# Optimization experiments

Hardware: AMD Instinct MI355X
Metric: run time of the kernel (lower is better)

Reference implementation:

```python
import jax, jax.numpy as jnp
import numpy as np

N, E = 20000, 320000
D_IN, HID, HEADS, OUT = 256, 64, 8, 64
K1 = int(np.ceil(0.75 * N))   # 15000 nodes after pool1
K2 = int(np.ceil(0.75 * K1))  # 11250 nodes after pool2
NEG = -1e30


def setup_inputs():
    key = jax.random.key(0)
    ks = jax.random.split(key, 24)
    s = 0.1
    rn = lambda k, shape: jax.random.normal(k, shape, jnp.float32) * s
    HH = HEADS * HID  # 512
    p = {}
    p["x"] = jax.random.normal(ks[0], (N, D_IN), jnp.float32)
    p["edge_index"] = jax.random.randint(ks[1], (2, E), 0, N, dtype=jnp.int32)
    # gat1: GATv2Conv(D_IN -> HID, heads=HEADS), concat output dim HH
    p["g1_wl"] = rn(ks[2], (D_IN, HH)); p["g1_wr"] = rn(ks[3], (D_IN, HH))
    p["g1_att"] = rn(ks[4], (HEADS, HID)); p["g1_b"] = jnp.zeros((HH,), jnp.float32)
    # pool1 scoring GNN: GATConv(HH -> 1, heads=1) + SelectTopK weight
    p["p1_w"] = rn(ks[5], (HH, 1)); p["p1_asrc"] = rn(ks[6], (1,)); p["p1_adst"] = rn(ks[7], (1,))
    p["p1_b"] = jnp.zeros((1,), jnp.float32); p["p1_sel"] = rn(ks[8], (1,)) + 0.5
    # gat2: GATv2Conv(HH -> HID, heads=1)
    p["g2_wl"] = rn(ks[9], (HH, HID)); p["g2_wr"] = rn(ks[10], (HH, HID))
    p["g2_att"] = rn(ks[11], (1, HID)); p["g2_b"] = jnp.zeros((HID,), jnp.float32)
    # pool2 scoring GNN: GATConv(HID -> 1)
    p["p2_w"] = rn(ks[12], (HID, 1)); p["p2_asrc"] = rn(ks[13], (1,)); p["p2_adst"] = rn(ks[14], (1,))
    p["p2_b"] = jnp.zeros((1,), jnp.float32); p["p2_sel"] = rn(ks[15], (1,)) + 0.5
    # MLP head
    p["l1_w"] = rn(ks[16], (2 * HH, HH)); p["l1_b"] = jnp.zeros((HH,), jnp.float32)
    d2 = OUT * (HEADS // 2); d3 = OUT * (HEADS // 4)
    p["l2_w"] = rn(ks[17], (HH, d2)); p["l2_b"] = jnp.zeros((d2,), jnp.float32)
    p["l3_w"] = rn(ks[18], (d2, d3)); p["l3_b"] = jnp.zeros((d3,), jnp.float32)
    p["l4_w"] = rn(ks[19], (d3, 2)); p["l4_b"] = jnp.zeros((2,), jnp.float32)
    return p


def _seg_softmax(e, dst, valid, n):
    # numerically stable segment softmax over destination nodes; invalid edges -> 0
    e = jnp.where(valid[:, None], e, NEG)
    m = jax.ops.segment_max(e, dst, num_segments=n)
    ex = jnp.exp(e - m[dst])
    ex = jnp.where(valid[:, None], ex, 0.0)
    den = jax.ops.segment_sum(ex, dst, num_segments=n)
    return ex / den[dst]


def gatv2(x, src, dst, valid, wl, wr, att, b):
    # GATv2Conv: score = att . LeakyReLU(Wl x_src + Wr x_dst), segment softmax, concat heads
    n = x.shape[0]
    h, c = att.shape
    xl = (x @ wl).reshape(n, h, c)
    xr = (x @ wr).reshape(n, h, c)
    loop = jnp.arange(n, dtype=src.dtype)  # add_self_loops=True
    s = jnp.concatenate([src, loop]); d = jnp.concatenate([dst, loop])
    v = jnp.concatenate([valid, jnp.ones((n,), bool)])
    m = jax.nn.leaky_relu(xl[s] + xr[d], 0.2)          # [E', H, C]
    e = jnp.einsum("ehc,hc->eh", m, att)               # [E', H]
    a = _seg_softmax(e, d, v, n)
    out = jax.ops.segment_sum(a[..., None] * xl[s], d, num_segments=n)
    return out.reshape(n, h * c) + b


def gat_score(x, src, dst, valid, w, asrc, adst, b):
    # GATConv(in -> 1, heads=1): per-node scalar projection score
    n = x.shape[0]
    xl = x @ w                                          # [n, 1]
    al = (xl * asrc).sum(-1); ar = (xl * adst).sum(-1)  # [n]
    loop = jnp.arange(n, dtype=src.dtype)
    s = jnp.concatenate([src, loop]); d = jnp.concatenate([dst, loop])
    v = jnp.concatenate([valid, jnp.ones((n,), bool)])
    e = jax.nn.leaky_relu(al[s] + ar[d], 0.2)[:, None]
    a = _seg_softmax(e, d, v, n)
    return jax.ops.segment_sum(a * xl[s], d, num_segments=n) + b


def sag_pool(x, src, dst, valid, k, w, asrc, adst, b, sel_w):
    # SAGPooling: GNN score -> tanh -> top-k -> x[perm]*score, edge filtering via mask
    attn = gat_score(x, src, dst, valid, w, asrc, adst, b)           # [n, 1]
    score = jnp.tanh((attn * sel_w).sum(-1) / jnp.linalg.norm(sel_w))  # SelectTopK
    vals, perm = jax.lax.top_k(score, k)
    xp = x[perm] * vals[:, None]
    new_id = jnp.full((x.shape[0],), -1, src.dtype).at[perm].set(jnp.arange(k, dtype=src.dtype))
    s2, d2 = new_id[src], new_id[dst]
    v2 = valid & (s2 >= 0) & (d2 >= 0)
    return xp, jnp.where(v2, s2, 0), jnp.where(v2, d2, 0), v2


def _forward(x, edge_index, g1_wl, g1_wr, g1_att, g1_b, p1_w, p1_asrc, p1_adst, p1_b, p1_sel,
             g2_wl, g2_wr, g2_att, g2_b, p2_w, p2_asrc, p2_adst, p2_b, p2_sel,
             l1_w, l1_b, l2_w, l2_b, l3_w, l3_b, l4_w, l4_b):
    src, dst = edge_index[0], edge_index[1]
    valid = jnp.ones((src.shape[0],), bool)
    h = jax.nn.relu(gatv2(x, src, dst, valid, g1_wl, g1_wr, g1_att, g1_b))
    h, s1, d1, v1 = sag_pool(h, src, dst, valid, K1, p1_w, p1_asrc, p1_adst, p1_b, p1_sel)
    # single graph -> global pools are plain reductions over nodes
    x1 = jnp.concatenate([h.max(0, keepdims=True), h.mean(0, keepdims=True)], axis=1)
    h2 = jax.nn.relu(gatv2(h, s1, d1, v1, g2_wl, g2_wr, g2_att, g2_b))
    h2, _, _, _ = sag_pool(h2, s1, d1, v1, K2, p2_w, p2_asrc, p2_adst, p2_b, p2_sel)
    gmax = jnp.tile(h2.max(0, keepdims=True), (1, HEADS))
    gmean = jnp.tile(h2.mean(0, keepdims=True), (1, HEADS))
    z = x1 + jnp.concatenate([gmax, gmean], axis=1)
    z = jax.nn.relu(z @ l1_w + l1_b)   # dropout is identity at eval
    z = jax.nn.relu(z @ l2_w + l2_b)
    z = jax.nn.relu(z @ l3_w + l3_b)
    logits = z @ l4_w + l4_b
    return logits, jax.nn.softmax(logits, axis=-1)


def reference(x, edge_index, g1_wl, g1_wr, g1_att, g1_b, p1_w, p1_asrc, p1_adst, p1_b, p1_sel,
              g2_wl, g2_wr, g2_att, g2_b, p2_w, p2_asrc, p2_adst, p2_b, p2_sel,
              l1_w, l1_b, l2_w, l2_b, l3_w, l3_b, l4_w, l4_b):
    return _forward(x, edge_index, g1_wl, g1_wr, g1_att, g1_b, p1_w, p1_asrc, p1_adst, p1_b, p1_sel,
                    g2_wl, g2_wr, g2_att, g2_b, p2_w, p2_asrc, p2_adst, p2_b, p2_sel,
                    l1_w, l1_b, l2_w, l2_b, l3_w, l3_b, l4_w, l4_b)
```

## Files before the change

### kernel.cpp

```cpp
#include <hip/hip_runtime.h>
#include <math.h>

#define N_NODES 20000
#define E_EDGES 320000
#define DIN     256
#define HHD     512
#define HIDD    64
#define NHEADS  8
#define K1N     15000
#define K2N     11250

typedef unsigned short u16;
typedef __attribute__((ext_vector_type(8))) short bf16x8;
typedef __attribute__((ext_vector_type(4))) float f32x4;

static inline int cdiv(long long a, long long b) { return (int)((a + b - 1) / b); }

__device__ __forceinline__ void atomicMaxF(float* addr, float val) {
  int* ai = (int*)addr;
  int old = __float_as_int(*addr);
  while (__int_as_float(old) < val) {
    int assumed = old;
    old = atomicCAS(ai, assumed, __float_as_int(val));
    if (old == assumed) break;
  }
}

__device__ __forceinline__ u16 f2bf(float x) {
  unsigned u = __float_as_uint(x);
  return (u16)((u + 0x7FFFu + ((u >> 16) & 1u)) >> 16);
}
__device__ __forceinline__ float bfval(u16 b) { return __uint_as_float(((unsigned)b) << 16); }

__global__ void init_all(int* deg1, int* rank1, float* pools) {
  int i = blockIdx.x * blockDim.x + threadIdx.x;
  if (i < N_NODES) deg1[i] = 0;
  else if (i < 2 * N_NODES) rank1[i - N_NODES] = 0;
  else {
    int idx = i - 2 * N_NODES;
    if (idx < 1152)
      pools[idx] = (idx < 512 || (idx >= 1024 && idx < 1088)) ? -INFINITY : 0.f;
  }
}

__global__ void conv_fused(const float* __restrict__ A, const int* __restrict__ perm,
                           const float* __restrict__ scalev,
                           u16* __restrict__ ah, u16* __restrict__ al, int M, int K,
                           const float* __restrict__ w1, const float* __restrict__ w2,
                           u16* __restrict__ wh, u16* __restrict__ wl, int ncHalf,
                           int aBlocks) {
  if ((int)blockIdx.x < aBlocks) {
    long long i = (long long)blockIdx.x * blockDim.x + threadIdx.x;
    long long e0 = i * 4;
    if (e0 >= (long long)M * K) return;
    int row = (int)(e0 / K), col = (int)(e0 % K);
    int ar = perm ? perm[row] : row;
    float4 v = *(const float4*)(A + (size_t)ar * K + col);
    if (scalev) { float s = scalev[ar]; v.x *= s; v.y *= s; v.z *= s; v.w *= s; }
    u16 h0 = f2bf(v.x), h1 = f2bf(v.y), h2 = f2bf(v.z), h3 = f2bf(v.w);
    u16 l0 = f2bf(v.x - bfval(h0)), l1 = f2bf(v.y - bfval(h1));
    u16 l2 = f2bf(v.z - bfval(h2)), l3 = f2bf(v.w - bfval(h3));
    uint2 hp, lp;
    hp.x = (unsigned)h0 | ((unsigned)h1 << 16); hp.y = (unsigned)h2 | ((unsigned)h3 << 16);
    lp.x = (unsigned)l0 | ((unsigned)l1 << 16); lp.y = (unsigned)l2 | ((unsigned)l3 << 16);
    *(uint2*)(ah + e0) = hp;
    *(uint2*)(al + e0) = lp;
  } else {
    int i = (blockIdx.x - aBlocks) * blockDim.x + threadIdx.x;
    int NT = 2 * ncHalf;
    if (i >= NT * K) return;
    int n = i % NT, k = i / NT;
    float v = (n < ncHalf) ? w1[(size_t)k * ncHalf + n] : w2[(size_t)k * ncHalf + (n - ncHalf)];
    u16 h = f2bf(v);
    u16 l = f2bf(v - bfval(h));
    wh[(size_t)n * K + k] = h;
    wl[(size_t)n * K + k] = l;
  }
}

template<int BT>
__global__ __launch_bounds__(256) void gemm_bf16x3(const u16* __restrict__ ah,
                                                   const u16* __restrict__ al,
                                                   const u16* __restrict__ wh,
                                                   const u16* __restrict__ wl,
                                                   float* __restrict__ c1,
                                                   float* __restrict__ c2,
                                                   int M, int K, int ncHalf) {
  constexpr int F = BT / 32;
  __shared__ u16 Ah[BT][40], Al[BT][40], Bh[BT][40], Bl[BT][40];
  int tid = threadIdx.x;
  int lane = tid & 63, wid = tid >> 6;
  int wr = (wid >> 1) * (BT / 2), wc = (wid & 1) * (BT / 2);
  int brow = blockIdx.y * BT, bcol = blockIdx.x * BT;
  int fr = lane & 15, kg = lane >> 4;
  f32x4 acc[F][F];
#pragma unroll
  for (int i = 0; i < F; i++)
#pragma unroll
    for (int j = 0; j < F; j++) acc[i][j] = (f32x4){0.f, 0.f, 0.f, 0.f};

  for (int k0 = 0; k0 < K; k0 += 32) {
    constexpr int ITER = (BT * 32) / (256 * 8);
#pragma unroll
    for (int i = 0; i < ITER; i++) {
      int pos = tid + i * 256;
      int row = pos >> 2;
      int kc = (pos & 3) * 8;
      int gr = brow + row;
      float4 z = make_float4(0.f, 0.f, 0.f, 0.f);
      float4 vah = (gr < M) ? *(const float4*)(ah + (size_t)gr * K + k0 + kc) : z;
      float4 val = (gr < M) ? *(const float4*)(al + (size_t)gr * K + k0 + kc) : z;
      *(float4*)(&Ah[row][kc]) = vah;
      *(float4*)(&Al[row][kc]) = val;
      int gn = bcol + row;
      *(float4*)(&Bh[row][kc]) = *(const float4*)(wh + (size_t)gn * K + k0 + kc);
      *(float4*)(&Bl[row][kc]) = *(const float4*)(wl + (size_t)gn * K + k0 + kc);
    }
    __syncthreads();
    bf16x8 fa_h[F], fa_l[F], fb_h[F], fb_l[F];
#pragma unroll
    for (int t = 0; t < F; t++) {
      fa_h[t] = *(const bf16x8*)(&Ah[wr + t * 16 + fr][kg * 8]);
      fa_l[t] = *(const bf16x8*)(&Al[wr + t * 16 + fr][kg * 8]);
      fb_h[t] = *(const bf16x8*)(&Bh[wc + t * 16 + fr][kg * 8]);
      fb_l[t] = *(const bf16x8*)(&Bl[wc + t * 16 + fr][kg * 8]);
    }
#pragma unroll
    for (int i = 0; i < F; i++)
#pragma unroll
      for (int j = 0; j < F; j++) {
        acc[i][j] = __builtin_amdgcn_mfma_f32_16x16x32_bf16(fa_h[i], fb_h[j], acc[i][j], 0, 0, 0);
        acc[i][j] = __builtin_amdgcn_mfma_f32_16x16x32_bf16(fa_h[i], fb_l[j], acc[i][j], 0, 0, 0);
        acc[i][j] = __builtin_amdgcn_mfma_f32_16x16x32_bf16(fa_l[i], fb_h[j], acc[i][j], 0, 0, 0);
      }
    __syncthreads();
  }
#pragma unroll
  for (int i = 0; i < F; i++) {
    int r0 = brow + wr + i * 16 + kg * 4;
#pragma unroll
    for (int j = 0; j < F; j++) {
      int cg = bcol + wc + j * 16 + fr;
      float* cp = (cg < ncHalf) ? c1 : c2;
      int cc = (cg < ncHalf) ? cg : cg - ncHalf;
#pragma unroll
      for (int r = 0; r < 4; r++) {
        int gr = r0 + r;
        if (gr < M) cp[(size_t)gr * ncHalf + cc] = acc[i][j][r];
      }
    }
  }
}

__global__ void deg_count(const int* __restrict__ src, const int* __restrict__ dst,
                          const int* __restrict__ newid, int* __restrict__ deg,
                          int nloops) {
  int i = blockIdx.x * blockDim.x + threadIdx.x;
  if (i >= E_EDGES + nloops) return;
  int d;
  if (i < E_EDGES) {
    if (newid) {
      int s = newid[src[i]]; d = newid[dst[i]];
      if (s < 0 || d < 0) return;
    } else d = dst[i];
  } else d = i - E_EDGES;
  atomicAdd(&deg[d], 1);
}

__global__ __launch_bounds__(1024) void scan_excl(const int* deg, int* rowptr,
                                                  int* cursor, int n) {
  __shared__ int wsum[16];
  __shared__ int carry;
  int tid = threadIdx.x, lane = tid & 63, wid = tid >> 6;
  if (tid == 0) { carry = 0; rowptr[0] = 0; }
  __syncthreads();
  for (int base = 0; base < n; base += 1024) {
    int v = (base + tid < n) ? deg[base + tid] : 0;
    int s = v;
#pragma unroll
    for (int off = 1; off < 64; off <<= 1) {
      int t = __shfl_up(s, off);
      if (lane >= off) s += t;
    }
    if (lane == 63) wsum[wid] = s;
    __syncthreads();
    if (wid == 0) {
      int w = (lane < 16) ? wsum[lane] : 0;
#pragma unroll
      for (int off = 1; off < 16; off <<= 1) {
        int t = __shfl_up(w, off);
        if (lane >= off) w += t;
      }
      if (lane < 16) wsum[lane] = w;
    }
    __syncthreads();
    int incl = s + (wid > 0 ? wsum[wid - 1] : 0) + carry;
    if (base + tid < n) { rowptr[base + tid + 1] = incl; cursor[base + tid] = incl - v; }
    __syncthreads();
    if (tid == 1023) carry = incl;
    __syncthreads();
  }
}

__global__ void csr_scatter(const int* __restrict__ src, const int* __restrict__ dst,
                            const int* __restrict__ newid, int* __restrict__ cursor,
                            int* __restrict__ csr_s, int nloops) {
  int i = blockIdx.x * blockDim.x + threadIdx.x;
  if (i >= E_EDGES + nloops) return;
  int s, d;
  if (i < E_EDGES) {
    s = src[i]; d = dst[i];
    if (newid) {
      s = newid[s]; d = newid[d];
      if (s < 0 || d < 0) return;
    }
  } else s = d = i - E_EDGES;
  int pos = atomicAdd(&cursor[d], 1);
  csr_s[pos] = s;
}

__global__ __launch_bounds__(256) void gat1_fused(const int* __restrict__ rowptr,
                                                  const int* __restrict__ csr_s,
                                                  const float* __restrict__ xl,
                                                  const float* __restrict__ xr,
                                                  const float* __restrict__ att,
                                                  const float* __restrict__ bias,
                                                  const float* __restrict__ pw,
                                                  float* __restrict__ out,
                                                  float* __restrict__ xls) {
  int lane = threadIdx.x & 63;
  long long t = (long long)blockIdx.x * blockDim.x + threadIdx.x;
  int d = (int)(t >> 6);
  if (d >= N_NODES) return;
  int base = lane * 8;
  float4 a0 = *(const float4*)(att + base);
  float4 a1 = *(const float4*)(att + base + 4);
  const float* xrp = xr + (size_t)d * HHD + base;
  float4 r0 = *(const float4*)(xrp);
  float4 r1 = *(const float4*)(xrp + 4);
  float m = -INFINITY, den = 0.f;
  float acc[8] = {0.f, 0.f, 0.f, 0.f, 0.f, 0.f, 0.f, 0.f};
  int b0 = rowptr[d];
  int cnt = rowptr[d + 1] - b0;
  const int* sp = csr_s + b0;

  auto online = [&](float4 v0, float4 v1) {
    float p, tv;
    tv = v0.x + r0.x; tv = tv > 0.f ? tv : 0.2f * tv; p  = tv * a0.x;
    tv = v0.y + r0.y; tv = tv > 0.f ? tv : 0.2f * tv; p += tv * a0.y;
    tv = v0.z + r0.z; tv = tv > 0.f ? tv : 0.2f * tv; p += tv * a0.z;
    tv = v0.w + r0.w; tv = tv > 0.f ? tv : 0.2f * tv; p += tv * a0.w;
    tv = v1.x + r1.x; tv = tv > 0.f ? tv : 0.2f * tv; p += tv * a1.x;
    tv = v1.y + r1.y; tv = tv > 0.f ? tv : 0.2f * tv; p += tv * a1.y;
    tv = v1.z + r1.z; tv = tv > 0.f ? tv : 0.2f * tv; p += tv * a1.z;
    tv = v1.w + r1.w; tv = tv > 0.f ? tv : 0.2f * tv; p += tv * a1.w;
    p += __shfl_xor(p, 1); p += __shfl_xor(p, 2); p += __shfl_xor(p, 4);
    float nm = fmaxf(m, p);
    float w  = __expf(p - nm);
    float sc = __expf(m - nm);
    den = den * sc + w;
    acc[0] = acc[0] * sc + w * v0.x;
    acc[1] = acc[1] * sc + w * v0.y;
    acc[2] = acc[2] * sc + w * v0.z;
    acc[3] = acc[3] * sc + w * v0.w;
    acc[4] = acc[4] * sc + w * v1.x;
    acc[5] = acc[5] * sc + w * v1.y;
    acc[6] = acc[6] * sc + w * v1.z;
    acc[7] = acc[7] * sc + w * v1.w;
    m = nm;
  };

  float4 A0, A1, B0, B1, C0, C1, D0, D1;
  float4 zz = make_float4(0.f, 0.f, 0.f, 0.f);
  {
    const float* p0 = xl + (size_t)sp[0] * HHD + base;
    A0 = *(const float4*)p0; A1 = *(const float4*)(p0 + 4);
  }
  B0 = zz; B1 = zz; C0 = zz; C1 = zz; D0 = zz; D1 = zz;
  if (cnt > 1) { const float* p = xl + (size_t)sp[1] * HHD + base; B0 = *(const float4*)p; B1 = *(const float4*)(p + 4); }
  if (cnt > 2) { const float* p = xl + (size_t)sp[2] * HHD + base; C0 = *(const float4*)p; C1 = *(const float4*)(p + 4); }
  if (cnt > 3) { const float* p = xl + (size_t)sp[3] * HHD + base; D0 = *(const float4*)p; D1 = *(const float4*)(p + 4); }
  int j = 0;
  for (; j + 4 <= cnt; j += 4) {
    float4 v0 = A0, v1 = A1;
    if (j + 4 < cnt) { const float* p = xl + (size_t)sp[j + 4] * HHD + base; A0 = *(const float4*)p; A1 = *(const float4*)(p + 4); }
    online(v0, v1);
    v0 = B0; v1 = B1;
    if (j + 5 < cnt) { const float* p = xl + (size_t)sp[j + 5] * HHD + base; B0 = *(const float4*)p; B1 = *(const float4*)(p + 4); }
    online(v0, v1);
    v0 = C0; v1 = C1;
    if (j + 6 < cnt) { const float* p = xl + (size_t)sp[j + 6] * HHD + base; C0 = *(const float4*)p; C1 = *(const float4*)(p + 4); }
    online(v0, v1);
    v0 = D0; v1 = D1;
    if (j + 7 < cnt) { const float* p = xl + (size_t)sp[j + 7] * HHD + base; D0 = *(const float4*)p; D1 = *(const float4*)(p + 4); }
    online(v0, v1);
  }
  if (j < cnt) {
    online(A0, A1);
    if (j + 1 < cnt) {
      online(B0, B1);
      if (j + 2 < cnt) online(C0, C1);
    }
  }

  float inv = 1.f / den;
  float4 b0v = *(const float4*)(bias + base);
  float4 b1v = *(const float4*)(bias + base + 4);
  float o[8];
  o[0] = acc[0] * inv + b0v.x; o[1] = acc[1] * inv + b0v.y;
  o[2] = acc[2] * inv + b0v.z; o[3] = acc[3] * inv + b0v.w;
  o[4] = acc[4] * inv + b1v.x; o[5] = acc[5] * inv + b1v.y;
  o[6] = acc[6] * inv + b1v.z; o[7] = acc[7] * inv + b1v.w;
#pragma unroll
  for (int k = 0; k < 8; k++) o[k] = o[k] > 0.f ? o[k] : 0.f;
  float* op = out + (size_t)d * HHD + base;
  *(float4*)(op)     = make_float4(o[0], o[1], o[2], o[3]);
  *(float4*)(op + 4) = make_float4(o[4], o[5], o[6], o[7]);
  float4 w0 = *(const float4*)(pw + base);
  float4 w1 = *(const float4*)(pw + base + 4);
  float sdot = o[0]*w0.x + o[1]*w0.y + o[2]*w0.z + o[3]*w0.w
             + o[4]*w1.x + o[5]*w1.y + o[6]*w1.z + o[7]*w1.w;
#pragma unroll
  for (int off = 32; off > 0; off >>= 1) sdot += __shfl_xor(sdot, off);
  if (lane == 0) xls[d] = sdot;
}

__global__ __launch_bounds__(256) void gat2_fused(const int* __restrict__ rowptr,
                                                  const int* __restrict__ csr_s,
                                                  const float* __restrict__ xl,
                                                  const float* __restrict__ xr,
                                                  const float* __restrict__ att,
                                                  const float* __restrict__ bias,
                                                  const float* __restrict__ pw,
                                                  float* __restrict__ out,
                                                  float* __restrict__ xls, int n) {
  int lane = threadIdx.x & 63;
  long long t = (long long)blockIdx.x * blockDim.x + threadIdx.x;
  int d = (int)(t >> 6);
  if (d >= n) return;
  float av = att[lane];
  float rr = xr[(size_t)d * HIDD + lane];
  float m = -INFINITY, den = 0.f, acc = 0.f;
  int b0 = rowptr[d];
  int cnt = rowptr[d + 1] - b0;
  const int* sp = csr_s + b0;

  auto online = [&](float v) {
    float tv = v + rr; tv = tv > 0.f ? tv : 0.2f * tv;
    float p = tv * av;
#pragma unroll
    for (int off = 32; off > 0; off >>= 1) p += __shfl_xor(p, off);
    float nm = fmaxf(m, p);
    float w  = __expf(p - nm);
    float sc = __expf(m - nm);
    den = den * sc + w;
    acc = acc * sc + w * v;
    m = nm;
  };

  float vA = xl[(size_t)sp[0] * HIDD + lane];
  float vB = (cnt > 1) ? xl[(size_t)sp[1] * HIDD + lane] : 0.f;
  float vC = (cnt > 2) ? xl[(size_t)sp[2] * HIDD + lane] : 0.f;
  float vD = (cnt > 3) ? xl[(size_t)sp[3] * HIDD + lane] : 0.f;
  int j = 0;
  for (; j + 4 <= cnt; j += 4) {
    float v = vA;
    if (j + 4 < cnt) vA = xl[(size_t)sp[j + 4] * HIDD + lane];
    online(v);
    v = vB;
    if (j + 5 < cnt) vB = xl[(size_t)sp[j + 5] * HIDD + lane];
    online(v);
    v = vC;
    if (j + 6 < cnt) vC = xl[(size_t)sp[j + 6] * HIDD + lane];
    online(v);
    v = vD;
    if (j + 7 < cnt) vD = xl[(size_t)sp[j + 7] * HIDD + lane];
    online(v);
  }
  if (j < cnt) {
    online(vA);
    if (j + 1 < cnt) {
      online(vB);
      if (j + 2 < cnt) online(vC);
    }
  }

  float o = acc / den + bias[lane];
  o = o > 0.f ? o : 0.f;
  out[(size_t)d * HIDD + lane] = o;
  float sdot = o * pw[lane];
#pragma unroll
  for (int off = 32; off > 0; off >>= 1) sdot += __shfl_xor(sdot, off);
  if (lane == 0) xls[d] = sdot;
}

__global__ __launch_bounds__(256) void pool_score(const int* __restrict__ rowptr,
                                                  const int* __restrict__ csr_s,
                                                  const float* __restrict__ xls,
                                                  const float* __restrict__ asrc,
                                                  const float* __restrict__ adst,
                                                  const float* __restrict__ bias,
                                                  const float* __restrict__ sel,
                                                  float* __restrict__ score, int n) {
  int d = blockIdx.x * blockDim.x + threadIdx.x;
  if (d >= n) return;
  float as = asrc[0], ad = adst[0];
  float ar = xls[d] * ad;
  int b0 = rowptr[d];
  int cnt = rowptr[d + 1] - b0;
  const int* sp = csr_s + b0;
  float m = -INFINITY, den = 0.f, num = 0.f;
  auto upd = [&](float xs) {
    float e = xs * as + ar;
    e = e > 0.f ? e : 0.2f * e;
    float nm = fmaxf(m, e);
    float scv = __expf(m - nm);
    float ex = __expf(e - nm);
    den = den * scv + ex;
    num = num * scv + ex * xs;
    m = nm;
  };
  float xA = xls[sp[0]];
  float xB = (cnt > 1) ? xls[sp[1]] : 0.f;
  float xC = (cnt > 2) ? xls[sp[2]] : 0.f;
  float xD = (cnt > 3) ? xls[sp[3]] : 0.f;
  int j = 0;
  for (; j + 4 <= cnt; j += 4) {
    float x1 = xA;
    if (j + 4 < cnt) xA = xls[sp[j + 4]];
    upd(x1);
    float x2 = xB;
    if (j + 5 < cnt) xB = xls[sp[j + 5]];
    upd(x2);
    float x3 = xC;
    if (j + 6 < cnt) xC = xls[sp[j + 6]];
    upd(x3);
    float x4 = xD;
    if (j + 7 < cnt) xD = xls[sp[j + 7]];
    upd(x4);
  }
  if (j < cnt) {
    upd(xA);
    if (j + 1 < cnt) {
      upd(xB);
      if (j + 2 < cnt) upd(xC);
    }
  }
  float attn = num / den + bias[0];
  float sv = sel[0];
  score[d] = tanhf(attn * sv / fabsf(sv));
}

#define TK_CHUNK 512
__global__ __launch_bounds__(256) void topk_count(const float* __restrict__ score,
                                                  int* __restrict__ rank, int n,
                                                  int* __restrict__ zbuf, int zn) {
  __shared__ float sc[TK_CHUNK];
  if (zbuf) {
    long long fid = ((long long)blockIdx.y * gridDim.x + blockIdx.x) * 256 + threadIdx.x;
    if (fid < zn) zbuf[fid] = 0;
  }
  int i = blockIdx.x * 256 + threadIdx.x;
  int base = blockIdx.y * TK_CHUNK;
  int cnt = min(TK_CHUNK, n - base);
  for (int j = threadIdx.x; j < cnt; j += 256) sc[j] = score[base + j];
  __syncthreads();
  if (i >= n) return;
  float si = score[i];
  int r = 0;
  for (int j = 0; j < cnt; j++) {
    float sj = sc[j];
    r += (sj > si) || ((sj == si) && ((base + j) < i));
  }
  if (r) atomicAdd(&rank[i], r);
}

__global__ void topk_assign(const int* __restrict__ rank, int* __restrict__ newid,
                            int* __restrict__ perm, int n, int k) {
  int i = blockIdx.x * blockDim.x + threadIdx.x;
  if (i < n) {
    int r = rank[i];
    newid[i] = (r < k) ? r : -1;
    if (r < k) perm[r] = i;
  }
}

__global__ __launch_bounds__(256) void col_pool_conv(const float* __restrict__ X,
                                                     const int* __restrict__ perm,
                                                     const float* __restrict__ scalev,
                                                     float* __restrict__ omax,
                                                     float* __restrict__ osum,
                                                     u16* __restrict__ ah, u16* __restrict__ al,
                                                     const float* __restrict__ w1,
                                                     const float* __restrict__ w2,
                                                     u16* __restrict__ wh, u16* __restrict__ wl,
                                                     int cpBlocks) {
  int tid = threadIdx.x;
  if ((int)blockIdx.x < cpBlocks) {
    float mx[2] = {-INFINITY, -INFINITY};
    float sm[2] = {0.f, 0.f};
    int rpb = (K1N + cpBlocks - 1) / cpBlocks;
    int rbeg = blockIdx.x * rpb;
    int rend = min(K1N, rbeg + rpb);
    for (int r = rbeg; r < rend; r++) {
      int orow = perm[r];
      float sc = scalev[orow];
      const float* row = X + (size_t)orow * HHD;
#pragma unroll
      for (int sg = 0; sg < 2; sg++) {
        int c = sg * 256 + tid;
        float v = row[c] * sc;
        mx[sg] = fmaxf(mx[sg], v);
        sm[sg] += v;
        u16 h = f2bf(v);
        u16 l = f2bf(v - bfval(h));
        ah[(size_t)r * HHD + c] = h;
        al[(size_t)r * HHD + c] = l;
      }
    }
    if (rbeg < rend) {
#pragma unroll
      for (int sg = 0; sg < 2; sg++) {
        int c = sg * 256 + tid;
        atomicMaxF(&omax[c], mx[sg]);
        atomicAdd(&osum[c], sm[sg]);
      }
    }
  } else {
    int i = (blockIdx.x - cpBlocks) * 256 + tid;
    const int NT = 2 * HIDD;
    if (i >= NT * HHD) return;
    int n = i % NT, k = i / NT;
    float v = (n < HIDD) ? w1[(size_t)k * HIDD + n] : w2[(size_t)k * HIDD + (n - HIDD)];
    u16 h = f2bf(v);
    u16 l = f2bf(v - bfval(h));
    wh[(size_t)n * HHD + k] = h;
    wl[(size_t)n * HHD + k] = l;
  }
}

__global__ __launch_bounds__(256) void col_pool(const float* __restrict__ X,
                                                const int* __restrict__ perm,
                                                const float* __restrict__ scalev,
                                                int rows, int C,
                                                float* __restrict__ omax, float* __restrict__ osum) {
  int tid = threadIdx.x;
  float mx = -INFINITY, sm = 0.f;
  int rpb = (rows + gridDim.x - 1) / gridDim.x;
  int rbeg = blockIdx.x * rpb;
  int rend = min(rows, rbeg + rpb);
  for (int r = rbeg; r < rend; r++) {
    int orow = perm[r];
    float sc = scalev[orow];
    int c = tid;
    if (c < C) {
      float v = X[(size_t)orow * C + c] * sc;
      mx = fmaxf(mx, v);
      sm += v;
    }
  }
  if (rbeg < rend && tid < C) {
    atomicMaxF(&omax[tid], mx);
    atomicAdd(&osum[tid], sm);
  }
}

__global__ __launch_bounds__(256) void mlp_l1(const float* __restrict__ pools,
                                              const float* __restrict__ w1,
                                              const float* __restrict__ b1,
                                              float* __restrict__ z1out) {
  __shared__ float z[1024];
  __shared__ float red[16][17];
  int t = threadIdx.x;
  for (int i = t; i < 1024; i += 256) {
    float xv = (i < 512) ? pools[i] : pools[i] * (1.f / K1N);
    float gv = (i < 512) ? pools[1024 + (i & 63)] : pools[1088 + (i & 63)] * (1.f / K2N);
    z[i] = xv + gv;
  }
  __syncthreads();
  int jl = t & 15, ch = t >> 4;
  int j = blockIdx.x * 16 + jl;
  float p = 0.f;
  for (int k = ch * 64; k < ch * 64 + 64; k++) p += z[k] * w1[(size_t)k * 512 + j];
  red[ch][jl] = p;
  __syncthreads();
  if (t < 16) {
    float s = b1[blockIdx.x * 16 + t];
    for (int c = 0; c < 16; c++) s += red[c][t];
    z1out[blockIdx.x * 16 + t] = s > 0.f ? s : 0.f;
  }
}

__global__ __launch_bounds__(256) void mlp_tail(const float* __restrict__ z1,
                                                const float* __restrict__ w2, const float* __restrict__ b2,
                                                const float* __restrict__ w3, const float* __restrict__ b3,
                                                const float* __restrict__ w4, const float* __restrict__ b4,
                                                float* __restrict__ out) {
  __shared__ float z2[256], z3[128], lg[2];
  int t = threadIdx.x;
  {
    float acc = b2[t];
    for (int k = 0; k < 512; k++) acc += z1[k] * w2[(size_t)k * 256 + t];
    z2[t] = acc > 0.f ? acc : 0.f;
  }
  __syncthreads();
  if (t < 128) {
    float acc = b3[t];
    for (int k = 0; k < 256; k++) acc += z2[k] * w3[(size_t)k * 128 + t];
    z3[t] = acc > 0.f ? acc : 0.f;
  }
  __syncthreads();
  if (t < 2) {
    float acc = b4[t];
    for (int k = 0; k < 128; k++) acc += z3[k] * w4[2 * k + t];
    lg[t] = acc;
  }
  __syncthreads();
  if (t == 0) {
    float m = fmaxf(lg[0], lg[1]);
    float e0 = __expf(lg[0] - m), e1 = __expf(lg[1] - m);
    float s = e0 + e1;
    out[0] = lg[0]; out[1] = lg[1];
    out[2] = e0 / s; out[3] = e1 / s;
  }
}

extern "C" void kernel_launch(void* const* d_in, const int* in_sizes, int n_in,
                              void* d_out, int out_size, void* d_ws, size_t ws_size,
                              hipStream_t stream) {
  const float* x       = (const float*)d_in[0];
  const int*   ei      = (const int*)d_in[1];
  const float* g1_wl   = (const float*)d_in[2];
  const float* g1_wr   = (const float*)d_in[3];
  const float* g1_att  = (const float*)d_in[4];
  const float* g1_b    = (const float*)d_in[5];
  const float* p1_w    = (const float*)d_in[6];
  const float* p1_asrc = (const float*)d_in[7];
  const float* p1_adst = (const float*)d_in[8];
  const float* p1_b    = (const float*)d_in[9];
  const float* p1_sel  = (const float*)d_in[10];
  const float* g2_wl   = (const float*)d_in[11];
  const float* g2_wr   = (const float*)d_in[12];
  const float* g2_att  = (const float*)d_in[13];
  const float* g2_b    = (const float*)d_in[14];
  const float* p2_w    = (const float*)d_in[15];
  const float* p2_asrc = (const float*)d_in[16];
  const float* p2_adst = (const float*)d_in[17];
  const float* p2_b    = (const float*)d_in[18];
  const float* p2_sel  = (const float*)d_in[19];
  const float* l1_w    = (const float*)d_in[20];
  const float* l1_b    = (const float*)d_in[21];
  const float* l2_w    = (const float*)d_in[22];
  const float* l2_b    = (const float*)d_in[23];
  const float* l3_w    = (const float*)d_in[24];
  const float* l3_b    = (const float*)d_in[25];
  const float* l4_w    = (const float*)d_in[26];
  const float* l4_b    = (const float*)d_in[27];

  const int* src = ei;
  const int* dst = ei + E_EDGES;

  if (ws_size < (size_t)33440000 * 4) return;
  float* ws  = (float*)d_ws;
  float* xl1 = ws;
  float* xr1 = ws + 10240000;
  float* h1  = ws + 20480000;
  float* aux = ws + 30720000;

  int*   csr_s1   = (int*)aux;
  int*   rowptr1  = (int*)(aux + 340000);
  int*   deg1     = (int*)(aux + 360064);
  int*   rank1    = (int*)(aux + 380064);
  int*   newid1   = (int*)(aux + 400064);
  float* xls1     = aux + 420064;
  float* scr1     = aux + 440064;
  float* pools    = aux + 460064;
  float* x1max    = pools;
  float* x1sum    = pools + 512;
  float* g2max    = pools + 1024;
  float* g2sum    = pools + 1088;
  int*   perm1    = (int*)(aux + 461248);
  float* z1       = aux + 481248;

  u16* ah1 = (u16*)h1;
  u16* al1 = ah1 + 5120000;
  u16* wh1 = al1 + 5120000;
  u16* wl1 = wh1 + 262144;

  u16* ah2 = (u16*)xl1;
  u16* al2 = ah2 + 7680000;
  u16* wh2 = al2 + 7680000;
  u16* wl2 = wh2 + 65536;

  float* a2 = xr1;
  float* xl2      = a2;
  float* xr2      = a2 + 960000;
  float* h2       = a2 + 1920000;
  int*   csr_s2   = (int*)(a2 + 2880000);
  int*   rowptr2  = (int*)(a2 + 3215000);
  int*   deg2     = (int*)(a2 + 3230016);
  int*   rank2    = (int*)(a2 + 3245016);
  int*   newid2   = (int*)(a2 + 3260016);
  float* xls2     = a2 + 3275016;
  float* scr2     = a2 + 3290016;
  int*   perm2    = (int*)(a2 + 3305016);

  dim3 b256(256);
  const int E1 = E_EDGES + N_NODES;
  const int E2 = E_EDGES + K1N;

  init_all<<<cdiv(2 * N_NODES + 1152, 256), b256, 0, stream>>>(deg1, rank1, pools);
  deg_count<<<cdiv(E1, 256), b256, 0, stream>>>(src, dst, nullptr, deg1, N_NODES);
  scan_excl<<<1, 1024, 0, stream>>>(deg1, rowptr1, deg1, N_NODES);
  csr_scatter<<<cdiv(E1, 256), b256, 0, stream>>>(src, dst, nullptr, deg1, csr_s1, N_NODES);

  {
    int aBlocks = cdiv((long long)N_NODES * DIN / 4, 256);
    int wBlocks = cdiv(2 * HHD * DIN, 256);
    conv_fused<<<aBlocks + wBlocks, b256, 0, stream>>>(
        x, nullptr, nullptr, ah1, al1, N_NODES, DIN, g1_wl, g1_wr, wh1, wl1, HHD, aBlocks);
  }
  gemm_bf16x3<128><<<dim3(2 * HHD / 128, cdiv(N_NODES, 128)), b256, 0, stream>>>(
      ah1, al1, wh1, wl1, xl1, xr1, N_NODES, DIN, HHD);
  gat1_fused<<<cdiv((long long)N_NODES * 64, 256), b256, 0, stream>>>(
      rowptr1, csr_s1, xl1, xr1, g1_att, g1_b, p1_w, h1, xls1);

  pool_score<<<cdiv(N_NODES, 256), b256, 0, stream>>>(rowptr1, csr_s1, xls1,
                                                      p1_asrc, p1_adst, p1_b, p1_sel, scr1, N_NODES);
  topk_count<<<dim3(cdiv(N_NODES, 256), cdiv(N_NODES, TK_CHUNK)), b256, 0, stream>>>(
      scr1, rank1, N_NODES, deg2, 30000);
  topk_assign<<<cdiv(N_NODES, 256), b256, 0, stream>>>(rank1, newid1, perm1, N_NODES, K1N);
  {
    int cpBlocks = 256;
    int wBlocks = cdiv(2 * HIDD * HHD, 256);
    col_pool_conv<<<cpBlocks + wBlocks, b256, 0, stream>>>(
        h1, perm1, scr1, x1max, x1sum, ah2, al2, g2_wl, g2_wr, wh2, wl2, cpBlocks);
  }

  deg_count<<<cdiv(E2, 256), b256, 0, stream>>>(src, dst, newid1, deg2, K1N);
  scan_excl<<<1, 1024, 0, stream>>>(deg2, rowptr2, deg2, K1N);
  csr_scatter<<<cdiv(E2, 256), b256, 0, stream>>>(src, dst, newid1, deg2, csr_s2, K1N);

  gemm_bf16x3<64><<<dim3(2 * HIDD / 64, cdiv(K1N, 64)), b256, 0, stream>>>(
      ah2, al2, wh2, wl2, xl2, xr2, K1N, HHD, HIDD);
  gat2_fused<<<cdiv((long long)K1N * 64, 256), b256, 0, stream>>>(
      rowptr2, csr_s2, xl2, xr2, g2_att, g2_b, p2_w, h2, xls2, K1N);

  pool_score<<<cdiv(K1N, 256), b256, 0, stream>>>(rowptr2, csr_s2, xls2,
                                                  p2_asrc, p2_adst, p2_b, p2_sel, scr2, K1N);
  topk_count<<<dim3(cdiv(K1N, 256), cdiv(K1N, TK_CHUNK)), b256, 0, stream>>>(
      scr2, rank2, K1N, nullptr, 0);
  topk_assign<<<cdiv(K1N, 256), b256, 0, stream>>>(rank2, newid2, perm2, K1N, K2N);
  col_pool<<<128, b256, 0, stream>>>(h2, perm2, scr2, K2N, HIDD, g2max, g2sum);

  mlp_l1<<<32, b256, 0, stream>>>(pools, l1_w, l1_b, z1);
  mlp_tail<<<1, b256, 0, stream>>>(z1, l2_w, l2_b, l3_w, l3_b, l4_w, l4_b, (float*)d_out);
}
```

Before: 550.4 us.

## Rebalance GAT aggregation: two waves per node in gat1, four nodes per wave in gat2

gat1 now splits each destination node's 512 channels across two wavefronts, with each lane handling 4 channels instead of 8. The pool-score dot product is combined across the two waves with an atomicAdd into xls1, which is now zeroed in init_all. gat2 packs four nodes per wavefront, with 16 lanes per node each reading a float4, replacing one node per wave with scalar loads, and uses a shallower 2-deep prefetch. The aim is more parallelism and memory-level concurrency in gat1 and better lane utilisation and vectorised gathers in gat2. The cost is an extra atomic and duplicated index and edge-loop work in gat1, and more lane divergence from differing node degrees within a gat2 wave.

```diff
diff --git a/kernel.cpp b/kernel.cpp
--- a/kernel.cpp
+++ b/kernel.cpp
@@ -32,12 +32,13 @@
 }
 __device__ __forceinline__ float bfval(u16 b) { return __uint_as_float(((unsigned)b) << 16); }
 
-__global__ void init_all(int* deg1, int* rank1, float* pools) {
+__global__ void init_all(int* deg1, int* rank1, float* xls1, float* pools) {
   int i = blockIdx.x * blockDim.x + threadIdx.x;
   if (i < N_NODES) deg1[i] = 0;
   else if (i < 2 * N_NODES) rank1[i - N_NODES] = 0;
+  else if (i < 3 * N_NODES) xls1[i - 2 * N_NODES] = 0.f;
   else {
-    int idx = i - 2 * N_NODES;
+    int idx = i - 3 * N_NODES;
     if (idx < 1152)
       pools[idx] = (idx < 512 || (idx >= 1024 && idx < 1088)) ? -INFINITY : 0.f;
   }
@@ -230,99 +231,77 @@
                                                   float* __restrict__ xls) {
   int lane = threadIdx.x & 63;
   long long t = (long long)blockIdx.x * blockDim.x + threadIdx.x;
-  int d = (int)(t >> 6);
+  int gw = (int)(t >> 6);
+  int d = gw >> 1;
   if (d >= N_NODES) return;
-  int base = lane * 8;
-  float4 a0 = *(const float4*)(att + base);
-  float4 a1 = *(const float4*)(att + base + 4);
-  const float* xrp = xr + (size_t)d * HHD + base;
-  float4 r0 = *(const float4*)(xrp);
-  float4 r1 = *(const float4*)(xrp + 4);
+  int cbase = (gw & 1) * 256 + lane * 4;
+  float4 av = *(const float4*)(att + cbase);
+  float4 rv = *(const float4*)(xr + (size_t)d * HHD + cbase);
   float m = -INFINITY, den = 0.f;
-  float acc[8] = {0.f, 0.f, 0.f, 0.f, 0.f, 0.f, 0.f, 0.f};
+  float4 acc = make_float4(0.f, 0.f, 0.f, 0.f);
   int b0 = rowptr[d];
   int cnt = rowptr[d + 1] - b0;
   const int* sp = csr_s + b0;
 
-  auto online = [&](float4 v0, float4 v1) {
+  auto online = [&](float4 v) {
     float p, tv;
-    tv = v0.x + r0.x; tv = tv > 0.f ? tv : 0.2f * tv; p  = tv * a0.x;
-    tv = v0.y + r0.y; tv = tv > 0.f ? tv : 0.2f * tv; p += tv * a0.y;
-    tv = v0.z + r0.z; tv = tv > 0.f ? tv : 0.2f * tv; p += tv * a0.z;
-    tv = v0.w + r0.w; tv = tv > 0.f ? tv : 0.2f * tv; p += tv * a0.w;
-    tv = v1.x + r1.x; tv = tv > 0.f ? tv : 0.2f * tv; p += tv * a1.x;
-    tv = v1.y + r1.y; tv = tv > 0.f ? tv : 0.2f * tv; p += tv * a1.y;
-    tv = v1.z + r1.z; tv = tv > 0.f ? tv : 0.2f * tv; p += tv * a1.z;
-    tv = v1.w + r1.w; tv = tv > 0.f ? tv : 0.2f * tv; p += tv * a1.w;
-    p += __shfl_xor(p, 1); p += __shfl_xor(p, 2); p += __shfl_xor(p, 4);
+    tv = v.x + rv.x; tv = tv > 0.f ? tv : 0.2f * tv; p  = tv * av.x;
+    tv = v.y + rv.y; tv = tv > 0.f ? tv : 0.2f * tv; p += tv * av.y;
+    tv = v.z + rv.z; tv = tv > 0.f ? tv : 0.2f * tv; p += tv * av.z;
+    tv = v.w + rv.w; tv = tv > 0.f ? tv : 0.2f * tv; p += tv * av.w;
+    p += __shfl_xor(p, 1); p += __shfl_xor(p, 2); p += __shfl_xor(p, 4); p += __shfl_xor(p, 8);
     float nm = fmaxf(m, p);
     float w  = __expf(p - nm);
     float sc = __expf(m - nm);
     den = den * sc + w;
-    acc[0] = acc[0] * sc + w * v0.x;
-    acc[1] = acc[1] * sc + w * v0.y;
-    acc[2] = acc[2] * sc + w * v0.z;
-    acc[3] = acc[3] * sc + w * v0.w;
-    acc[4] = acc[4] * sc + w * v1.x;
-    acc[5] = acc[5] * sc + w * v1.y;
-    acc[6] = acc[6] * sc + w * v1.z;
-    acc[7] = acc[7] * sc + w * v1.w;
+    acc.x = acc.x * sc + w * v.x;
+    acc.y = acc.y * sc + w * v.y;
+    acc.z = acc.z * sc + w * v.z;
+    acc.w = acc.w * sc + w * v.w;
     m = nm;
   };
 
-  float4 A0, A1, B0, B1, C0, C1, D0, D1;
   float4 zz = make_float4(0.f, 0.f, 0.f, 0.f);
-  {
-    const float* p0 = xl + (size_t)sp[0] * HHD + base;
-    A0 = *(const float4*)p0; A1 = *(const float4*)(p0 + 4);
-  }
-  B0 = zz; B1 = zz; C0 = zz; C1 = zz; D0 = zz; D1 = zz;
-  if (cnt > 1) { const float* p = xl + (size_t)sp[1] * HHD + base; B0 = *(const float4*)p; B1 = *(const float4*)(p + 4); }
-  if (cnt > 2) { const float* p = xl + (size_t)sp[2] * HHD + base; C0 = *(const float4*)p; C1 = *(const float4*)(p + 4); }
-  if (cnt > 3) { const float* p = xl + (size_t)sp[3] * HHD + base; D0 = *(const float4*)p; D1 = *(const float4*)(p + 4); }
+  float4 A = *(const float4*)(xl + (size_t)sp[0] * HHD + cbase);
+  float4 B = (cnt > 1) ? *(const float4*)(xl + (size_t)sp[1] * HHD + cbase) : zz;
+  float4 C = (cnt > 2) ? *(const float4*)(xl + (size_t)sp[2] * HHD + cbase) : zz;
+  float4 D = (cnt > 3) ? *(const float4*)(xl + (size_t)sp[3] * HHD + cbase) : zz;
   int j = 0;
   for (; j + 4 <= cnt; j += 4) {
-    float4 v0 = A0, v1 = A1;
-    if (j + 4 < cnt) { const float* p = xl + (size_t)sp[j + 4] * HHD + base; A0 = *(const float4*)p; A1 = *(const float4*)(p + 4); }
-    online(v0, v1);
-    v0 = B0; v1 = B1;
-    if (j + 5 < cnt) { const float* p = xl + (size_t)sp[j + 5] * HHD + base; B0 = *(const float4*)p; B1 = *(const float4*)(p + 4); }
-    online(v0, v1);
-    v0 = C0; v1 = C1;
-    if (j + 6 < cnt) { const float* p = xl + (size_t)sp[j + 6] * HHD + base; C0 = *(const float4*)p; C1 = *(const float4*)(p + 4); }
-    online(v0, v1);
-    v0 = D0; v1 = D1;
-    if (j + 7 < cnt) { const float* p = xl + (size_t)sp[j + 7] * HHD + base; D0 = *(const float4*)p; D1 = *(const float4*)(p + 4); }
-    online(v0, v1);
+    float4 v = A;
+    if (j + 4 < cnt) A = *(const float4*)(xl + (size_t)sp[j + 4] * HHD + cbase);
+    online(v);
+    v = B;
+    if (j + 5 < cnt) B = *(const float4*)(xl + (size_t)sp[j + 5] * HHD + cbase);
+    online(v);
+    v = C;
+    if (j + 6 < cnt) C = *(const float4*)(xl + (size_t)sp[j + 6] * HHD + cbase);
+    online(v);
+    v = D;
+    if (j + 7 < cnt) D = *(const float4*)(xl + (size_t)sp[j + 7] * HHD + cbase);
+    online(v);
   }
   if (j < cnt) {
-    online(A0, A1);
+    online(A);
     if (j + 1 < cnt) {
-      online(B0, B1);
-      if (j + 2 < cnt) online(C0, C1);
+      online(B);
+      if (j + 2 < cnt) online(C);
     }
   }
 
   float inv = 1.f / den;
-  float4 b0v = *(const float4*)(bias + base);
-  float4 b1v = *(const float4*)(bias + base + 4);
-  float o[8];
-  o[0] = acc[0] * inv + b0v.x; o[1] = acc[1] * inv + b0v.y;
-  o[2] = acc[2] * inv + b0v.z; o[3] = acc[3] * inv + b0v.w;
-  o[4] = acc[4] * inv + b1v.x; o[5] = acc[5] * inv + b1v.y;
-  o[6] = acc[6] * inv + b1v.z; o[7] = acc[7] * inv + b1v.w;
-#pragma unroll
-  for (int k = 0; k < 8; k++) o[k] = o[k] > 0.f ? o[k] : 0.f;
-  float* op = out + (size_t)d * HHD + base;
-  *(float4*)(op)     = make_float4(o[0], o[1], o[2], o[3]);
-  *(float4*)(op + 4) = make_float4(o[4], o[5], o[6], o[7]);
-  float4 w0 = *(const float4*)(pw + base);
-  float4 w1 = *(const float4*)(pw + base + 4);
-  float sdot = o[0]*w0.x + o[1]*w0.y + o[2]*w0.z + o[3]*w0.w
-             + o[4]*w1.x + o[5]*w1.y + o[6]*w1.z + o[7]*w1.w;
+  float4 bv = *(const float4*)(bias + cbase);
+  float4 o;
+  o.x = acc.x * inv + bv.x; o.y = acc.y * inv + bv.y;
+  o.z = acc.z * inv + bv.z; o.w = acc.w * inv + bv.w;
+  o.x = o.x > 0.f ? o.x : 0.f; o.y = o.y > 0.f ? o.y : 0.f;
+  o.z = o.z > 0.f ? o.z : 0.f; o.w = o.w > 0.f ? o.w : 0.f;
+  *(float4*)(out + (size_t)d * HHD + cbase) = o;
+  float4 wv = *(const float4*)(pw + cbase);
+  float sdot = o.x * wv.x + o.y * wv.y + o.z * wv.z + o.w * wv.w;
 #pragma unroll
   for (int off = 32; off > 0; off >>= 1) sdot += __shfl_xor(sdot, off);
-  if (lane == 0) xls[d] = sdot;
+  if (lane == 0) atomicAdd(&xls[d], sdot);
 }
 
 __global__ __launch_bounds__(256) void gat2_fused(const int* __restrict__ rowptr,
@@ -335,63 +314,65 @@
                                                   float* __restrict__ out,
                                                   float* __restrict__ xls, int n) {
   int lane = threadIdx.x & 63;
+  int grp = lane >> 4, li = lane & 15;
   long long t = (long long)blockIdx.x * blockDim.x + threadIdx.x;
-  int d = (int)(t >> 6);
+  int wv = (int)(t >> 6);
+  int d = wv * 4 + grp;
   if (d >= n) return;
-  float av = att[lane];
-  float rr = xr[(size_t)d * HIDD + lane];
-  float m = -INFINITY, den = 0.f, acc = 0.f;
+  int c0 = li * 4;
+  float4 av = *(const float4*)(att + c0);
+  float4 rv = *(const float4*)(xr + (size_t)d * HIDD + c0);
+  float m = -INFINITY, den = 0.f;
+  float4 acc = make_float4(0.f, 0.f, 0.f, 0.f);
   int b0 = rowptr[d];
   int cnt = rowptr[d + 1] - b0;
   const int* sp = csr_s + b0;
 
-  auto online = [&](float v) {
-    float tv = v + rr; tv = tv > 0.f ? tv : 0.2f * tv;
-    float p = tv * av;
-#pragma unroll
-    for (int off = 32; off > 0; off >>= 1) p += __shfl_xor(p, off);
+  auto online = [&](float4 v) {
+    float p, tv;
+    tv = v.x + rv.x; tv = tv > 0.f ? tv : 0.2f * tv; p  = tv * av.x;
+    tv = v.y + rv.y; tv = tv > 0.f ? tv : 0.2f * tv; p += tv * av.y;
+    tv = v.z + rv.z; tv = tv > 0.f ? tv : 0.2f * tv; p += tv * av.z;
+    tv = v.w + rv.w; tv = tv > 0.f ? tv : 0.2f * tv; p += tv * av.w;
+    p += __shfl_xor(p, 1); p += __shfl_xor(p, 2); p += __shfl_xor(p, 4); p += __shfl_xor(p, 8);
     float nm = fmaxf(m, p);
     float w  = __expf(p - nm);
     float sc = __expf(m - nm);
     den = den * sc + w;
-    acc = acc * sc + w * v;
+    acc.x = acc.x * sc + w * v.x;
+    acc.y = acc.y * sc + w * v.y;
+    acc.z = acc.z * sc + w * v.z;
+    acc.w = acc.w * sc + w * v.w;
     m = nm;
   };
 
-  float vA = xl[(size_t)sp[0] * HIDD + lane];
-  float vB = (cnt > 1) ? xl[(size_t)sp[1] * HIDD + lane] : 0.f;
-  float vC = (cnt > 2) ? xl[(size_t)sp[2] * HIDD + lane] : 0.f;
-  float vD = (cnt > 3) ? xl[(size_t)sp[3] * HIDD + lane] : 0.f;
+  float4 zz = make_float4(0.f, 0.f, 0.f, 0.f);
+  float4 A = *(const float4*)(xl + (size_t)sp[0] * HIDD + c0);
+  float4 B = (cnt > 1) ? *(const float4*)(xl + (size_t)sp[1] * HIDD + c0) : zz;
   int j = 0;
-  for (; j + 4 <= cnt; j += 4) {
-    float v = vA;
-    if (j + 4 < cnt) vA = xl[(size_t)sp[j + 4] * HIDD + lane];
+  for (; j + 2 <= cnt; j += 2) {
+    float4 v = A;
+    if (j + 2 < cnt) A = *(const float4*)(xl + (size_t)sp[j + 2] * HIDD + c0);
     online(v);
-    v = vB;
-    if (j + 5 < cnt) vB = xl[(size_t)sp[j + 5] * HIDD + lane];
+    v = B;
+    if (j + 3 < cnt) B = *(const float4*)(xl + (size_t)sp[j + 3] * HIDD + c0);
     online(v);
-    v = vC;
-    if (j + 6 < cnt) vC = xl[(size_t)sp[j + 6] * HIDD + lane];
-    online(v);
-    v = vD;
-    if (j + 7 < cnt) vD = xl[(size_t)sp[j + 7] * HIDD + lane];
-    online(v);
-  }
-  if (j < cnt) {
-    online(vA);
-    if (j + 1 < cnt) {
-      online(vB);
-      if (j + 2 < cnt) online(vC);
-    }
-  }
-
-  float o = acc / den + bias[lane];
-  o = o > 0.f ? o : 0.f;
-  out[(size_t)d * HIDD + lane] = o;
-  float sdot = o * pw[lane];
-#pragma unroll
-  for (int off = 32; off > 0; off >>= 1) sdot += __shfl_xor(sdot, off);
-  if (lane == 0) xls[d] = sdot;
+  }
+  if (j < cnt) online(A);
+
+  float inv = 1.f / den;
+  float4 bv = *(const float4*)(bias + c0);
+  float4 o;
+  o.x = acc.x * inv + bv.x; o.y = acc.y * inv + bv.y;
+  o.z = acc.z * inv + bv.z; o.w = acc.w * inv + bv.w;
+  o.x = o.x > 0.f ? o.x : 0.f; o.y = o.y > 0.f ? o.y : 0.f;
+  o.z = o.z > 0.f ? o.z : 0.f; o.w = o.w > 0.f ? o.w : 0.f;
+  *(float4*)(out + (size_t)d * HIDD + c0) = o;
+  float4 wv4 = *(const float4*)(pw + c0);
+  float sdot = o.x * wv4.x + o.y * wv4.y + o.z * wv4.z + o.w * wv4.w;
+  sdot += __shfl_xor(sdot, 1); sdot += __shfl_xor(sdot, 2);
+  sdot += __shfl_xor(sdot, 4); sdot += __shfl_xor(sdot, 8);
+  if (li == 0) xls[d] = sdot;
 }
 
 __global__ __launch_bounds__(256) void pool_score(const int* __restrict__ rowptr,
@@ -709,7 +690,7 @@
   const int E1 = E_EDGES + N_NODES;
   const int E2 = E_EDGES + K1N;
 
-  init_all<<<cdiv(2 * N_NODES + 1152, 256), b256, 0, stream>>>(deg1, rank1, pools);
+  init_all<<<cdiv(3 * N_NODES + 1152, 256), b256, 0, stream>>>(deg1, rank1, xls1, pools);
   deg_count<<<cdiv(E1, 256), b256, 0, stream>>>(src, dst, nullptr, deg1, N_NODES);
   scan_excl<<<1, 1024, 0, stream>>>(deg1, rowptr1, deg1, N_NODES);
   csr_scatter<<<cdiv(E1, 256), b256, 0, stream>>>(src, dst, nullptr, deg1, csr_s1, N_NODES);
@@ -722,7 +703,7 @@
   }
   gemm_bf16x3<128><<<dim3(2 * HHD / 128, cdiv(N_NODES, 128)), b256, 0, stream>>>(
       ah1, al1, wh1, wl1, xl1, xr1, N_NODES, DIN, HHD);
-  gat1_fused<<<cdiv((long long)N_NODES * 64, 256), b256, 0, stream>>>(
+  gat1_fused<<<cdiv((long long)N_NODES * 128, 256), b256, 0, stream>>>(
       rowptr1, csr_s1, xl1, xr1, g1_att, g1_b, p1_w, h1, xls1);
 
   pool_score<<<cdiv(N_NODES, 256), b256, 0, stream>>>(rowptr1, csr_s1, xls1,
@@ -743,7 +724,7 @@
 
   gemm_bf16x3<64><<<dim3(2 * HIDD / 64, cdiv(K1N, 64)), b256, 0, stream>>>(
       ah2, al2, wh2, wl2, xl2, xr2, K1N, HHD, HIDD);
-  gat2_fused<<<cdiv((long long)K1N * 64, 256), b256, 0, stream>>>(
+  gat2_fused<<<cdiv((long long)K1N * 16, 256), b256, 0, stream>>>(
       rowptr2, csr_s2, xl2, xr2, g2_att, g2_b, p2_w, h2, xls2, K1N);
 
   pool_score<<<cdiv(K1N, 256), b256, 0, stream>>>(rowptr2, csr_s2, xls2,
```

Result: no change. 553.6 us (+0.6%).
